# Performance work log

Hardware: AMD Instinct MI355X
Metric: run time of the kernel (lower is better)

The kernel has to match this reference:

```python
import jax, jax.numpy as jnp
import numpy as np

D_MODEL = 1024
NHEAD = 16
HEAD_DIM = D_MODEL // NHEAD
ROPE_BASE = 10000.0


def _rope_freq(T, head_dim):
    half = head_dim // 2
    pos = jnp.arange(T, dtype=jnp.float32)
    idx = jnp.arange(half, dtype=jnp.float32)
    freq_div = ROPE_BASE ** (2.0 * idx / head_dim)
    return pos[:, None] / freq_div[None, :]  # [T, half]


def _rope_rotate(x, cos, sin):
    # x: [B, H, T, d]; cos/sin: [T, d//2]
    half = x.shape[-1] // 2
    xl, xr = x[..., :half], x[..., half:]
    c = cos[None, None]
    s = sin[None, None]
    return jnp.concatenate([xl * c - xr * s, xl * s + xr * c], axis=-1)


def setup_inputs() -> dict:
    key = jax.random.key(0)
    ks = jax.random.split(key, 12)
    B, T = 2, 2048
    sd = 1.0 / np.sqrt(D_MODEL)
    inp = {
        "query": jax.random.normal(ks[0], (B, T, D_MODEL), jnp.float32),
        "key": jax.random.normal(ks[1], (B, T, D_MODEL), jnp.float32),
        "value": jax.random.normal(ks[2], (B, T, D_MODEL), jnp.float32),
        "frac": jax.random.uniform(ks[3], (B, T), jnp.float32),
        # Linear weights stored [in, out] (torch W.T)
        "Wq": jax.random.normal(ks[4], (D_MODEL, D_MODEL), jnp.float32) * sd,
        "Wk": jax.random.normal(ks[5], (D_MODEL, D_MODEL), jnp.float32) * sd,
        "Wv": jax.random.normal(ks[6], (D_MODEL, D_MODEL), jnp.float32) * sd,
        "Wo": jax.random.normal(ks[7], (D_MODEL, D_MODEL), jnp.float32) * sd,
        "bq": jnp.zeros((D_MODEL,), jnp.float32),
        "bk": jnp.zeros((D_MODEL,), jnp.float32),
        "bv": jnp.zeros((D_MODEL,), jnp.float32),
        "bo": jnp.zeros((D_MODEL,), jnp.float32),
        "alpha_pos": jax.random.normal(ks[8], (NHEAD,), jnp.float32) * 0.1,
        "alpha_neg": jax.random.normal(ks[9], (NHEAD,), jnp.float32) * 0.1,
    }
    return inp


def reference(query, key, value, frac, Wq, Wk, Wv, Wo, bq, bk, bv, bo, alpha_pos, alpha_neg):
    B, T, dm = query.shape
    H, hd = NHEAD, HEAD_DIM
    scale = hd ** -0.5

    def split_heads(x):  # [B,T,dm] -> [B,H,T,hd]
        return x.reshape(B, T, H, hd).transpose(0, 2, 1, 3)

    Q = split_heads(query @ Wq + bq)
    K = split_heads(key @ Wk + bk)
    V = split_heads(value @ Wv + bv)

    freq = _rope_freq(T, hd)
    cos, sin = jnp.cos(freq), jnp.sin(freq)
    Q = _rope_rotate(Q, cos, sin)
    K = _rope_rotate(K, cos, sin)

    scores = jnp.einsum("bhqd,bhkd->bhqk", Q, K) * scale  # [B,H,T,T]

    # data-dependent stoichiometric bias
    D = frac[:, None, :] - frac[:, :, None]  # [B,T,T], D[b,i,j] = frac_j - frac_i
    D_pos = jax.nn.relu(D)
    D_neg = -jax.nn.relu(-D)
    bias = (alpha_pos[None, :, None, None] * D_pos[:, None] +
            alpha_neg[None, :, None, None] * D_neg[:, None])  # [B,H,T,T]
    scores = scores + bias

    probs = jax.nn.softmax(scores, axis=-1)
    out = jnp.einsum("bhqk,bhkd->bhqd", probs, V)  # [B,H,T,hd]
    out = out.transpose(0, 2, 1, 3).reshape(B, T, dm)
    return out @ Wo + bo
```

## Files before the change

kernel.cpp:

```cpp
#include <hip/hip_runtime.h>


typedef unsigned short u16;
typedef __bf16 bf8v __attribute__((ext_vector_type(8)));
typedef __bf16 bf4v __attribute__((ext_vector_type(4)));
typedef float f32x4 __attribute__((ext_vector_type(4)));

#define D_MODEL 1024
#define T_SEQ   2048
#define NHEAD   16
#define HDIM    64
#define BATCH   2
#define M_TOT   (BATCH * T_SEQ)
#define LOG2E   1.4426950408889634f

__device__ __forceinline__ void gl2lds16(const u16* g, u16* l) {
  __builtin_amdgcn_global_load_lds(
      (__attribute__((address_space(1))) void*)g,
      (__attribute__((address_space(3))) void*)l, 16, 0, 0);
}

__global__ __launch_bounds__(256) void k_convert_x(
    const float* __restrict__ q, const float* __restrict__ k,
    const float* __restrict__ v, u16* __restrict__ out) {
  int z = blockIdx.y;
  const float* src = (z == 0) ? q : (z == 1) ? k : v;
  u16* dst = out + (size_t)z * (M_TOT * D_MODEL);
  int idx = (blockIdx.x * 256 + threadIdx.x) * 8;
  float4 a = *(const float4*)(src + idx);
  float4 b = *(const float4*)(src + idx + 4);
  bf8v o;
  o[0] = (__bf16)a.x; o[1] = (__bf16)a.y; o[2] = (__bf16)a.z; o[3] = (__bf16)a.w;
  o[4] = (__bf16)b.x; o[5] = (__bf16)b.y; o[6] = (__bf16)b.z; o[7] = (__bf16)b.w;
  *(bf8v*)(dst + idx) = o;
}

__global__ __launch_bounds__(256) void k_rope_table(float* __restrict__ ct,
                                                    float* __restrict__ st) {
  int idx = blockIdx.x * 256 + threadIdx.x;
  int t = idx >> 5, d = idx & 31;
  float ang = (float)t * powf(10000.0f, -(float)d * (1.0f / 32.0f));
  ct[idx] = cosf(ang);
  st[idx] = sinf(ang);
}

__global__ __launch_bounds__(256) void k_transpose_w(
    const float* __restrict__ Wq, const float* __restrict__ Wk,
    const float* __restrict__ Wv, const float* __restrict__ Wo,
    u16* __restrict__ WtB) {
  int z = blockIdx.z;
  const float* W = (z == 0) ? Wq : (z == 1) ? Wk : (z == 2) ? Wv : Wo;
  u16* Wt = WtB + (size_t)z * (D_MODEL * D_MODEL);
  __shared__ float tile[64 * 65];
  int n0 = blockIdx.x * 64, k0 = blockIdx.y * 64;
  int tid = threadIdx.x;
#pragma unroll
  for (int i = 0; i < 16; i++) {
    int idx = tid + i * 256;
    int r = idx >> 6, c = idx & 63;
    tile[c * 65 + r] = W[(size_t)(k0 + r) * D_MODEL + n0 + c];
  }
  __syncthreads();
#pragma unroll
  for (int i = 0; i < 16; i++) {
    int idx = tid + i * 256;
    int r = idx >> 6, c = idx & 63;
    ((__bf16*)Wt)[(size_t)(n0 + r) * D_MODEL + k0 + c] = (__bf16)tile[r * 65 + c];
  }
}

template <int BN>
__device__ __forceinline__ void gemm_core_t(const u16* __restrict__ A,
                                            const u16* __restrict__ Bt,
                                            u16* sA, u16* sB,
                                            f32x4 (&acc)[4][BN / 32],
                                            int m0, int n0) {
  const int K = D_MODEL;
  const int PB = BN * 32;
  int tid = threadIdx.x;
  int lane = tid & 63, wave = tid >> 6;
  int l15 = lane & 15, quad = lane >> 4;
  int wm = (wave >> 1) * 64, wn = (wave & 1) * (BN / 2);
  int r0 = tid >> 2, pcol0 = (tid & 3) * 8;
  int r1 = 64 + r0;
  const u16* A0 = A + (size_t)(m0 + r0) * K + pcol0;
  const u16* A1 = A + (size_t)(m0 + r1) * K + pcol0;
  const u16* B0 = Bt + (size_t)(n0 + r0) * K + pcol0;
  const u16* B1 = Bt + (size_t)(n0 + r1) * K + pcol0;
  u16* dA0 = sA + wave * 512;
  u16* dA1 = sA + 2048 + wave * 512;
  u16* dB0 = sB + wave * 512;
  u16* dB1 = sB + 2048 + wave * 512;
  for (int k0 = 0; k0 < K; k0 += 64) {
    __syncthreads();
    gl2lds16(A0 + k0, dA0);
    gl2lds16(A1 + k0, dA1);
    gl2lds16(A0 + k0 + 32, dA0 + 4096);
    gl2lds16(A1 + k0 + 32, dA1 + 4096);
    gl2lds16(B0 + k0, dB0);
    gl2lds16(B0 + k0 + 32, dB0 + PB);
    if (BN == 128) {
      gl2lds16(B1 + k0, dB1);
      gl2lds16(B1 + k0 + 32, dB1 + PB);
    }
    __syncthreads();
#pragma unroll
    for (int kh = 0; kh < 2; kh++) {
      bf8v af[4], bf[BN / 32];
#pragma unroll
      for (int i = 0; i < 4; i++)
        af[i] = *(const bf8v*)(sA + kh * 4096 + (wm + i * 16 + l15) * 32 + quad * 8);
#pragma unroll
      for (int i = 0; i < BN / 32; i++)
        bf[i] = *(const bf8v*)(sB + kh * PB + (wn + i * 16 + l15) * 32 + quad * 8);
#pragma unroll
      for (int mi = 0; mi < 4; mi++)
#pragma unroll
        for (int ni = 0; ni < BN / 32; ni++)
          acc[mi][ni] = __builtin_amdgcn_mfma_f32_16x16x32_bf16(
              af[mi], bf[ni], acc[mi][ni], 0, 0, 0);
    }
  }
}

__global__ __launch_bounds__(256) void k_gemm_qkv(
    const u16* __restrict__ Xb, const u16* __restrict__ WtB,
    const float* __restrict__ bq, const float* __restrict__ bk,
    const float* __restrict__ bv, const float* __restrict__ ctab,
    const float* __restrict__ stab, u16* __restrict__ OutB) {
  __shared__ __align__(16) u16 sA[128 * 64];
  __shared__ __align__(16) u16 sB[128 * 64];
  int z = blockIdx.z;
  const u16* A = Xb + (size_t)z * (M_TOT * D_MODEL);
  const u16* Bt = WtB + (size_t)z * (D_MODEL * D_MODEL);
  const float* bias = (z == 0) ? bq : (z == 1) ? bk : bv;
  u16* Out = OutB + (size_t)z * (M_TOT * D_MODEL);
  int m0 = blockIdx.y * 128, n0 = blockIdx.x * 128;
  f32x4 acc[4][4] = {};
  gemm_core_t<128>(A, Bt, sA, sB, acc, m0, n0);

  int tid = threadIdx.x, lane = tid & 63, wave = tid >> 6;
  int l15 = lane & 15, quad = lane >> 4;
  int wm = (wave >> 1) * 64, wn = (wave & 1) * 64;
  float bvv[4];
#pragma unroll
  for (int ni = 0; ni < 4; ni++) bvv[ni] = bias[n0 + wn + ni * 16 + l15];
  bool rope = (z < 2);
  float qs = (z == 0) ? 0.125f * LOG2E : 1.0f;
#pragma unroll
  for (int mi = 0; mi < 4; mi++) {
#pragma unroll
    for (int r = 0; r < 4; r++) {
      int m = m0 + wm + mi * 16 + quad * 4 + r;
      size_t ro = (size_t)m * D_MODEL + n0 + wn;
      if (rope) {
        int tl = m & (T_SEQ - 1);
#pragma unroll
        for (int ni = 0; ni < 2; ni++) {
          int d = ni * 16 + l15;
          float c = ctab[tl * 32 + d], s = stab[tl * 32 + d];
          float xl = acc[mi][ni][r] + bvv[ni];
          float xr = acc[mi][ni + 2][r] + bvv[ni + 2];
          ((__bf16*)Out)[ro + d] = (__bf16)((xl * c - xr * s) * qs);
          ((__bf16*)Out)[ro + d + 32] = (__bf16)((xl * s + xr * c) * qs);
        }
      } else {
#pragma unroll
        for (int ni = 0; ni < 4; ni++)
          ((__bf16*)Out)[ro + ni * 16 + l15] = (__bf16)(acc[mi][ni][r] + bvv[ni]);
      }
    }
  }
}

__global__ __launch_bounds__(256) void k_gemm_out(
    const u16* __restrict__ ctx, const u16* __restrict__ Wot,
    const float* __restrict__ bo, float* __restrict__ Cout) {
  __shared__ __align__(16) u16 sA[128 * 64];
  __shared__ __align__(16) u16 sB[64 * 64];
  int m0 = blockIdx.y * 128, n0 = blockIdx.x * 64;
  f32x4 acc[4][2] = {};
  gemm_core_t<64>(ctx, Wot, sA, sB, acc, m0, n0);
  int tid = threadIdx.x, lane = tid & 63, wave = tid >> 6;
  int l15 = lane & 15, quad = lane >> 4;
  int wm = (wave >> 1) * 64, wn = (wave & 1) * 32;
  float bvv[2];
#pragma unroll
  for (int ni = 0; ni < 2; ni++) bvv[ni] = bo[n0 + wn + ni * 16 + l15];
#pragma unroll
  for (int mi = 0; mi < 4; mi++)
#pragma unroll
    for (int r = 0; r < 4; r++) {
      size_t ro = (size_t)(m0 + wm + mi * 16 + quad * 4 + r) * D_MODEL + n0 + wn;
#pragma unroll
      for (int ni = 0; ni < 2; ni++)
        Cout[ro + ni * 16 + l15] = acc[mi][ni][r] + bvv[ni];
    }
}

__global__ __launch_bounds__(256) void k_v_transpose(const u16* __restrict__ Vtmp,
                                                     u16* __restrict__ Vb) {
  int bh = blockIdx.y;
  int b = bh >> 4, h = bh & 15;
  int t0 = blockIdx.x * 64;
  __shared__ u16 st[64 * 65];
  int tid = threadIdx.x;
#pragma unroll
  for (int i = 0; i < 16; i++) {
    int idx = tid + i * 256;
    int tt = idx >> 6, d = idx & 63;
    st[d * 65 + tt] = Vtmp[(size_t)(b * T_SEQ + t0 + tt) * D_MODEL + h * HDIM + d];
  }
  __syncthreads();
#pragma unroll
  for (int i = 0; i < 16; i++) {
    int idx = tid + i * 256;
    int d = idx >> 6, tt = idx & 63;
    Vb[((size_t)bh * HDIM + d) * T_SEQ + t0 + tt] = st[d * 65 + tt];
  }
}

__global__ __launch_bounds__(256) void k_attn(
    const u16* __restrict__ Qr, const u16* __restrict__ Kr,
    const u16* __restrict__ Vb, const float* __restrict__ frac,
    const float* __restrict__ alpha_pos, const float* __restrict__ alpha_neg,
    u16* __restrict__ ctx) {
  __shared__ __align__(16) u16 kT[2][64 * 64];
  __shared__ __align__(16) u16 vT[2][64 * 64];
  __shared__ __align__(16) u16 pT[4][2][16 * 72];
  int bh = blockIdx.y, b = bh >> 4, h = bh & 15;
  int q0 = blockIdx.x * 128;
  int tid = threadIdx.x, wave = tid >> 6, lane = tid & 63;
  int l15 = lane & 15, quad = lane >> 4;

  const u16* Kh = Kr + (size_t)b * T_SEQ * D_MODEL + h * HDIM;
  const u16* Vh = Vb + (size_t)bh * HDIM * T_SEQ;
  const float* fb = frac + b * T_SEQ;

  bf8v qf[2][2];
  float fq[2];
#pragma unroll
  for (int g = 0; g < 2; g++) {
    int qrow = q0 + wave * 32 + g * 16 + l15;
    const u16* qbase =
        Qr + (size_t)(b * T_SEQ + qrow) * D_MODEL + h * HDIM + quad * 8;
    qf[g][0] = *(const bf8v*)qbase;
    qf[g][1] = *(const bf8v*)(qbase + 32);
    fq[g] = fb[qrow];
  }
  float ap = alpha_pos[h] * LOG2E, an = alpha_neg[h] * LOG2E;
  bf8v onesv;
#pragma unroll
  for (int j = 0; j < 8; j++) onesv[j] = (__bf16)1.0f;
  f32x4 o[2][4] = {};
  f32x4 o_l[2] = {};
  u16* pw = (u16*)pT[wave];

  int p0 = tid, p1 = 256 + tid;
  int kr0 = p0 >> 3, gc0 = (p0 & 7) ^ (kr0 & 7);
  int kr1 = p1 >> 3, gc1 = (p1 & 7) ^ (kr1 & 7);
  const u16* kg0 = Kh + (size_t)kr0 * D_MODEL + gc0 * 8;
  const u16* kg1 = Kh + (size_t)kr1 * D_MODEL + gc1 * 8;
  const u16* vg0 = Vh + (size_t)kr0 * T_SEQ + gc0 * 8;
  const u16* vg1 = Vh + (size_t)kr1 * T_SEQ + gc1 * 8;
  int woff = wave * 512;

  auto stage = [&](int buf, int kbase) {
    gl2lds16(kg0 + (size_t)kbase * D_MODEL, kT[buf] + woff);
    gl2lds16(kg1 + (size_t)kbase * D_MODEL, kT[buf] + 2048 + woff);
    gl2lds16(vg0 + kbase, vT[buf] + woff);
    gl2lds16(vg1 + kbase, vT[buf] + 2048 + woff);
  };

  stage(0, 0);
  __syncthreads();

  for (int kt = 0; kt < T_SEQ / 64; kt++) {
    int kbase = kt * 64;
    int buf = kt & 1;
    if (kt + 1 < T_SEQ / 64) stage(buf ^ 1, kbase + 64);

    bf8v kf0[4], kf1[4];
    int x0 = (quad ^ (l15 & 7)) * 8;
#pragma unroll
    for (int nt = 0; nt < 4; nt++) {
      const u16* rb = kT[buf] + ((nt * 16 + l15) << 6);
      kf0[nt] = *(const bf8v*)(rb + x0);
      kf1[nt] = *(const bf8v*)(rb + (x0 ^ 32));
    }
    bf8v vf[2][4];
#pragma unroll
    for (int dt = 0; dt < 4; dt++) {
      const u16* rb = vT[buf] + ((dt * 16 + l15) << 6);
      vf[0][dt] = *(const bf8v*)(rb + x0);
      vf[1][dt] = *(const bf8v*)(rb + (x0 ^ 32));
    }
    f32x4 fk4[4];
#pragma unroll
    for (int nt = 0; nt < 4; nt++)
      fk4[nt] = *(const f32x4*)(fb + kbase + nt * 16 + quad * 4);

#pragma unroll
    for (int g = 0; g < 2; g++) {
      float fqg = fq[g];
      u16* pwg = pw + g * (16 * 72);
#pragma unroll
      for (int nt = 0; nt < 4; nt++) {
        f32x4 s = {};
        s = __builtin_amdgcn_mfma_f32_16x16x32_bf16(kf0[nt], qf[g][0], s, 0, 0, 0);
        s = __builtin_amdgcn_mfma_f32_16x16x32_bf16(kf1[nt], qf[g][1], s, 0, 0, 0);
        bf4v pk;
#pragma unroll
        for (int r = 0; r < 4; r++) {
          float dd = fk4[nt][r] - fqg;
          float sel = (dd >= 0.0f) ? ap : an;
          float p = __builtin_amdgcn_exp2f(fmaf(dd, sel, s[r]));
          pk[r] = (__bf16)p;
        }
        *(bf4v*)(pwg + l15 * 72 + nt * 16 + quad * 4) = pk;
      }
    }
    asm volatile("s_waitcnt lgkmcnt(0)" ::: "memory");

#pragma unroll
    for (int g = 0; g < 2; g++) {
      u16* pwg = pw + g * (16 * 72);
#pragma unroll
      for (int kc = 0; kc < 2; kc++) {
        bf8v pf = *(const bf8v*)(pwg + l15 * 72 + kc * 32 + quad * 8);
        o_l[g] = __builtin_amdgcn_mfma_f32_16x16x32_bf16(pf, onesv, o_l[g], 0, 0, 0);
#pragma unroll
        for (int dt = 0; dt < 4; dt++)
          o[g][dt] = __builtin_amdgcn_mfma_f32_16x16x32_bf16(pf, vf[kc][dt],
                                                             o[g][dt], 0, 0, 0);
      }
    }
    __syncthreads();
  }

#pragma unroll
  for (int g = 0; g < 2; g++) {
#pragma unroll
    for (int r = 0; r < 4; r++) {
      float linv = 1.0f / o_l[g][r];
      int qg = q0 + wave * 32 + g * 16 + quad * 4 + r;
      __bf16* orow = (__bf16*)(ctx + (size_t)(b * T_SEQ + qg) * D_MODEL + h * HDIM);
#pragma unroll
      for (int dt = 0; dt < 4; dt++)
        orow[dt * 16 + l15] = (__bf16)(o[g][dt][r] * linv);
    }
  }
}

extern "C" void kernel_launch(void* const* d_in, const int* in_sizes, int n_in,
                              void* d_out, int out_size, void* d_ws,
                              size_t ws_size, hipStream_t stream) {
  const float* q = (const float*)d_in[0];
  const float* k = (const float*)d_in[1];
  const float* v = (const float*)d_in[2];
  const float* frac = (const float*)d_in[3];
  const float* Wq = (const float*)d_in[4];
  const float* Wk = (const float*)d_in[5];
  const float* Wv = (const float*)d_in[6];
  const float* Wo = (const float*)d_in[7];
  const float* bq = (const float*)d_in[8];
  const float* bk = (const float*)d_in[9];
  const float* bv = (const float*)d_in[10];
  const float* bo = (const float*)d_in[11];
  const float* alpha_pos = (const float*)d_in[12];
  const float* alpha_neg = (const float*)d_in[13];

  char* ws = (char*)d_ws;
  u16* Xb = (u16*)(ws + 0);
  u16* Wt = (u16*)(ws + 25165824);
  u16* Qr = (u16*)(ws + 33554432);
  u16* Kr = (u16*)(ws + 41943040);
  u16* Vtmp = (u16*)(ws + 50331648);
  u16* Vb = (u16*)(ws + 58720256);
  float* ctab = (float*)(ws + 67108864);
  float* stab = (float*)(ws + 67371008);
  u16* ctx = Vtmp;
  u16* QKVout = Qr;

  k_convert_x<<<dim3(2048, 3), 256, 0, stream>>>(q, k, v, Xb);
  k_rope_table<<<dim3(256), 256, 0, stream>>>(ctab, stab);
  k_transpose_w<<<dim3(16, 16, 4), 256, 0, stream>>>(Wq, Wk, Wv, Wo, Wt);
  k_gemm_qkv<<<dim3(8, 32, 3), 256, 0, stream>>>(Xb, Wt, bq, bk, bv, ctab, stab,
                                                 QKVout);
  k_v_transpose<<<dim3(32, 32), 256, 0, stream>>>(Vtmp, Vb);
  k_attn<<<dim3(16, 32), 256, 0, stream>>>(Qr, Kr, Vb, frac, alpha_pos,
                                           alpha_neg, ctx);
  k_gemm_out<<<dim3(16, 32), 256, 0, stream>>>(ctx, Wt + 3 * 1048576, bo,
                                               (float*)d_out);
}
```

Baseline: 268.9 us.

## Merge prep kernels, double-buffer GEMM loads, fuse V transpose, shrink attention P buffer

Folds the input conversion, weight transpose and RoPE table kernels into one launch. The GEMM core is rewritten to double-buffer 32-wide K slices with async global-to-LDS loads, so the next slice's fetch overlaps the current slice's MFMAs and each step needs only one barrier. The V projection epilogue now writes V directly in the transposed per-head layout, which removes the separate transpose kernel but produces strided, uncoalesced 2-byte stores. The attention kernel uses one P scratch tile per wave instead of two, which adds an extra LDS wait per query group.

New measurement: 275.1 us. +2.3%, slower.

```diff
diff --git a/kernel.cpp b/kernel.cpp
--- a/kernel.cpp
+++ b/kernel.cpp
@@ -20,106 +20,104 @@
       (__attribute__((address_space(3))) void*)l, 16, 0, 0);
 }
 
-__global__ __launch_bounds__(256) void k_convert_x(
+__global__ __launch_bounds__(256) void k_prep(
     const float* __restrict__ q, const float* __restrict__ k,
-    const float* __restrict__ v, u16* __restrict__ out) {
-  int z = blockIdx.y;
-  const float* src = (z == 0) ? q : (z == 1) ? k : v;
-  u16* dst = out + (size_t)z * (M_TOT * D_MODEL);
-  int idx = (blockIdx.x * 256 + threadIdx.x) * 8;
-  float4 a = *(const float4*)(src + idx);
-  float4 b = *(const float4*)(src + idx + 4);
-  bf8v o;
-  o[0] = (__bf16)a.x; o[1] = (__bf16)a.y; o[2] = (__bf16)a.z; o[3] = (__bf16)a.w;
-  o[4] = (__bf16)b.x; o[5] = (__bf16)b.y; o[6] = (__bf16)b.z; o[7] = (__bf16)b.w;
-  *(bf8v*)(dst + idx) = o;
-}
-
-__global__ __launch_bounds__(256) void k_rope_table(float* __restrict__ ct,
-                                                    float* __restrict__ st) {
-  int idx = blockIdx.x * 256 + threadIdx.x;
-  int t = idx >> 5, d = idx & 31;
-  float ang = (float)t * powf(10000.0f, -(float)d * (1.0f / 32.0f));
-  ct[idx] = cosf(ang);
-  st[idx] = sinf(ang);
-}
-
-__global__ __launch_bounds__(256) void k_transpose_w(
-    const float* __restrict__ Wq, const float* __restrict__ Wk,
-    const float* __restrict__ Wv, const float* __restrict__ Wo,
-    u16* __restrict__ WtB) {
-  int z = blockIdx.z;
-  const float* W = (z == 0) ? Wq : (z == 1) ? Wk : (z == 2) ? Wv : Wo;
-  u16* Wt = WtB + (size_t)z * (D_MODEL * D_MODEL);
+    const float* __restrict__ v, const float* __restrict__ Wq,
+    const float* __restrict__ Wk, const float* __restrict__ Wv,
+    const float* __restrict__ Wo, u16* __restrict__ Xb, u16* __restrict__ WtB,
+    float* __restrict__ ct, float* __restrict__ st) {
   __shared__ float tile[64 * 65];
-  int n0 = blockIdx.x * 64, k0 = blockIdx.y * 64;
-  int tid = threadIdx.x;
-#pragma unroll
-  for (int i = 0; i < 16; i++) {
-    int idx = tid + i * 256;
-    int r = idx >> 6, c = idx & 63;
-    tile[c * 65 + r] = W[(size_t)(k0 + r) * D_MODEL + n0 + c];
-  }
-  __syncthreads();
-#pragma unroll
-  for (int i = 0; i < 16; i++) {
-    int idx = tid + i * 256;
-    int r = idx >> 6, c = idx & 63;
-    ((__bf16*)Wt)[(size_t)(n0 + r) * D_MODEL + k0 + c] = (__bf16)tile[r * 65 + c];
+  int bx = blockIdx.x, tid = threadIdx.x;
+  if (bx < 6144) {
+    int z = bx >> 11, xb = bx & 2047;
+    const float* src = (z == 0) ? q : (z == 1) ? k : v;
+    u16* dst = Xb + (size_t)z * (M_TOT * D_MODEL);
+    int idx = (xb * 256 + tid) * 8;
+    float4 a = *(const float4*)(src + idx);
+    float4 b = *(const float4*)(src + idx + 4);
+    bf8v o;
+    o[0] = (__bf16)a.x; o[1] = (__bf16)a.y; o[2] = (__bf16)a.z; o[3] = (__bf16)a.w;
+    o[4] = (__bf16)b.x; o[5] = (__bf16)b.y; o[6] = (__bf16)b.z; o[7] = (__bf16)b.w;
+    *(bf8v*)(dst + idx) = o;
+  } else if (bx < 7168) {
+    int idx2 = bx - 6144;
+    int z = idx2 >> 8, rem = idx2 & 255;
+    int k0 = (rem >> 4) * 64, n0 = (rem & 15) * 64;
+    const float* W = (z == 0) ? Wq : (z == 1) ? Wk : (z == 2) ? Wv : Wo;
+    u16* Wt = WtB + (size_t)z * (D_MODEL * D_MODEL);
+#pragma unroll
+    for (int i = 0; i < 16; i++) {
+      int idx = tid + i * 256;
+      int r = idx >> 6, c = idx & 63;
+      tile[c * 65 + r] = W[(size_t)(k0 + r) * D_MODEL + n0 + c];
+    }
+    __syncthreads();
+#pragma unroll
+    for (int i = 0; i < 16; i++) {
+      int idx = tid + i * 256;
+      int r = idx >> 6, c = idx & 63;
+      ((__bf16*)Wt)[(size_t)(n0 + r) * D_MODEL + k0 + c] = (__bf16)tile[r * 65 + c];
+    }
+  } else {
+    int idx = (bx - 7168) * 256 + tid;
+    int t = idx >> 5, d = idx & 31;
+    float ang = (float)t * powf(10000.0f, -(float)d * (1.0f / 32.0f));
+    ct[idx] = cosf(ang);
+    st[idx] = sinf(ang);
   }
 }
 
 template <int BN>
-__device__ __forceinline__ void gemm_core_t(const u16* __restrict__ A,
-                                            const u16* __restrict__ Bt,
-                                            u16* sA, u16* sB,
-                                            f32x4 (&acc)[4][BN / 32],
-                                            int m0, int n0) {
+__device__ __forceinline__ void gemm_core_db(const u16* __restrict__ A,
+                                             const u16* __restrict__ Bt,
+                                             u16* sA, u16* sB,
+                                             f32x4 (&acc)[4][BN / 32],
+                                             int m0, int n0) {
   const int K = D_MODEL;
-  const int PB = BN * 32;
   int tid = threadIdx.x;
   int lane = tid & 63, wave = tid >> 6;
   int l15 = lane & 15, quad = lane >> 4;
   int wm = (wave >> 1) * 64, wn = (wave & 1) * (BN / 2);
-  int r0 = tid >> 2, pcol0 = (tid & 3) * 8;
-  int r1 = 64 + r0;
-  const u16* A0 = A + (size_t)(m0 + r0) * K + pcol0;
-  const u16* A1 = A + (size_t)(m0 + r1) * K + pcol0;
-  const u16* B0 = Bt + (size_t)(n0 + r0) * K + pcol0;
-  const u16* B1 = Bt + (size_t)(n0 + r1) * K + pcol0;
+  int arow = tid >> 2, acol = (tid & 3) * 8;
+  const u16* Ap0 = A + (size_t)(m0 + arow) * K + acol;
+  const u16* Ap1 = Ap0 + (size_t)64 * K;
+  const u16* Bp0 = Bt + (size_t)(n0 + arow) * K + acol;
+  const u16* Bp1 = Bp0 + (size_t)64 * K;
   u16* dA0 = sA + wave * 512;
   u16* dA1 = sA + 2048 + wave * 512;
   u16* dB0 = sB + wave * 512;
   u16* dB1 = sB + 2048 + wave * 512;
-  for (int k0 = 0; k0 < K; k0 += 64) {
+
+  auto stage = [&](int buf, int k0) {
+    int oa = buf * (128 * 32);
+    int ob = buf * (BN * 32);
+    gl2lds16(Ap0 + k0, dA0 + oa);
+    gl2lds16(Ap1 + k0, dA1 + oa);
+    gl2lds16(Bp0 + k0, dB0 + ob);
+    if (BN == 128) gl2lds16(Bp1 + k0, dB1 + ob);
+  };
+
+  stage(0, 0);
+  __syncthreads();
+  for (int k0 = 0; k0 < K; k0 += 32) {
+    int buf = (k0 >> 5) & 1;
+    if (k0 + 32 < K) stage(buf ^ 1, k0 + 32);
+    const u16* bA = sA + buf * (128 * 32);
+    const u16* bB = sB + buf * (BN * 32);
+    bf8v af[4], bf[BN / 32];
+#pragma unroll
+    for (int i = 0; i < 4; i++)
+      af[i] = *(const bf8v*)(bA + (wm + i * 16 + l15) * 32 + quad * 8);
+#pragma unroll
+    for (int i = 0; i < BN / 32; i++)
+      bf[i] = *(const bf8v*)(bB + (wn + i * 16 + l15) * 32 + quad * 8);
+#pragma unroll
+    for (int mi = 0; mi < 4; mi++)
+#pragma unroll
+      for (int ni = 0; ni < BN / 32; ni++)
+        acc[mi][ni] = __builtin_amdgcn_mfma_f32_16x16x32_bf16(
+            af[mi], bf[ni], acc[mi][ni], 0, 0, 0);
     __syncthreads();
-    gl2lds16(A0 + k0, dA0);
-    gl2lds16(A1 + k0, dA1);
-    gl2lds16(A0 + k0 + 32, dA0 + 4096);
-    gl2lds16(A1 + k0 + 32, dA1 + 4096);
-    gl2lds16(B0 + k0, dB0);
-    gl2lds16(B0 + k0 + 32, dB0 + PB);
-    if (BN == 128) {
-      gl2lds16(B1 + k0, dB1);
-      gl2lds16(B1 + k0 + 32, dB1 + PB);
-    }
-    __syncthreads();
-#pragma unroll
-    for (int kh = 0; kh < 2; kh++) {
-      bf8v af[4], bf[BN / 32];
-#pragma unroll
-      for (int i = 0; i < 4; i++)
-        af[i] = *(const bf8v*)(sA + kh * 4096 + (wm + i * 16 + l15) * 32 + quad * 8);
-#pragma unroll
-      for (int i = 0; i < BN / 32; i++)
-        bf[i] = *(const bf8v*)(sB + kh * PB + (wn + i * 16 + l15) * 32 + quad * 8);
-#pragma unroll
-      for (int mi = 0; mi < 4; mi++)
-#pragma unroll
-        for (int ni = 0; ni < BN / 32; ni++)
-          acc[mi][ni] = __builtin_amdgcn_mfma_f32_16x16x32_bf16(
-              af[mi], bf[ni], acc[mi][ni], 0, 0, 0);
-    }
   }
 }
 
@@ -127,9 +125,10 @@
     const u16* __restrict__ Xb, const u16* __restrict__ WtB,
     const float* __restrict__ bq, const float* __restrict__ bk,
     const float* __restrict__ bv, const float* __restrict__ ctab,
-    const float* __restrict__ stab, u16* __restrict__ OutB) {
-  __shared__ __align__(16) u16 sA[128 * 64];
-  __shared__ __align__(16) u16 sB[128 * 64];
+    const float* __restrict__ stab, u16* __restrict__ OutB,
+    u16* __restrict__ Vb) {
+  __shared__ __align__(16) u16 sA[2][128 * 32];
+  __shared__ __align__(16) u16 sB[2][128 * 32];
   int z = blockIdx.z;
   const u16* A = Xb + (size_t)z * (M_TOT * D_MODEL);
   const u16* Bt = WtB + (size_t)z * (D_MODEL * D_MODEL);
@@ -137,7 +136,7 @@
   u16* Out = OutB + (size_t)z * (M_TOT * D_MODEL);
   int m0 = blockIdx.y * 128, n0 = blockIdx.x * 128;
   f32x4 acc[4][4] = {};
-  gemm_core_t<128>(A, Bt, sA, sB, acc, m0, n0);
+  gemm_core_db<128>(A, Bt, &sA[0][0], &sB[0][0], acc, m0, n0);
 
   int tid = threadIdx.x, lane = tid & 63, wave = tid >> 6;
   int l15 = lane & 15, quad = lane >> 4;
@@ -145,15 +144,15 @@
   float bvv[4];
 #pragma unroll
   for (int ni = 0; ni < 4; ni++) bvv[ni] = bias[n0 + wn + ni * 16 + l15];
-  bool rope = (z < 2);
-  float qs = (z == 0) ? 0.125f * LOG2E : 1.0f;
-#pragma unroll
-  for (int mi = 0; mi < 4; mi++) {
-#pragma unroll
-    for (int r = 0; r < 4; r++) {
-      int m = m0 + wm + mi * 16 + quad * 4 + r;
-      size_t ro = (size_t)m * D_MODEL + n0 + wn;
-      if (rope) {
+
+  if (z < 2) {
+    float qs = (z == 0) ? 0.125f * LOG2E : 1.0f;
+#pragma unroll
+    for (int mi = 0; mi < 4; mi++) {
+#pragma unroll
+      for (int r = 0; r < 4; r++) {
+        int m = m0 + wm + mi * 16 + quad * 4 + r;
+        size_t ro = (size_t)m * D_MODEL + n0 + wn;
         int tl = m & (T_SEQ - 1);
 #pragma unroll
         for (int ni = 0; ni < 2; ni++) {
@@ -164,23 +163,36 @@
           ((__bf16*)Out)[ro + d] = (__bf16)((xl * c - xr * s) * qs);
           ((__bf16*)Out)[ro + d + 32] = (__bf16)((xl * s + xr * c) * qs);
         }
-      } else {
-#pragma unroll
-        for (int ni = 0; ni < 4; ni++)
-          ((__bf16*)Out)[ro + ni * 16 + l15] = (__bf16)(acc[mi][ni][r] + bvv[ni]);
       }
     }
+  } else {
+    int hh = (n0 + wn) >> 6;
+    int mbase = m0 + wm;
+    int bb = mbase >> 11;
+    int tbase = mbase & (T_SEQ - 1);
+    u16* Vw = Vb + (size_t)(bb * NHEAD + hh) * HDIM * T_SEQ;
+#pragma unroll
+    for (int mi = 0; mi < 4; mi++)
+#pragma unroll
+      for (int r = 0; r < 4; r++) {
+        int t = tbase + mi * 16 + quad * 4 + r;
+#pragma unroll
+        for (int ni = 0; ni < 4; ni++) {
+          int d = ni * 16 + l15;
+          ((__bf16*)Vw)[(size_t)d * T_SEQ + t] = (__bf16)(acc[mi][ni][r] + bvv[ni]);
+        }
+      }
   }
 }
 
 __global__ __launch_bounds__(256) void k_gemm_out(
     const u16* __restrict__ ctx, const u16* __restrict__ Wot,
     const float* __restrict__ bo, float* __restrict__ Cout) {
-  __shared__ __align__(16) u16 sA[128 * 64];
-  __shared__ __align__(16) u16 sB[64 * 64];
+  __shared__ __align__(16) u16 sA[2][128 * 32];
+  __shared__ __align__(16) u16 sB[2][64 * 32];
   int m0 = blockIdx.y * 128, n0 = blockIdx.x * 64;
   f32x4 acc[4][2] = {};
-  gemm_core_t<64>(ctx, Wot, sA, sB, acc, m0, n0);
+  gemm_core_db<64>(ctx, Wot, &sA[0][0], &sB[0][0], acc, m0, n0);
   int tid = threadIdx.x, lane = tid & 63, wave = tid >> 6;
   int l15 = lane & 15, quad = lane >> 4;
   int wm = (wave >> 1) * 64, wn = (wave & 1) * 32;
@@ -196,28 +208,6 @@
       for (int ni = 0; ni < 2; ni++)
         Cout[ro + ni * 16 + l15] = acc[mi][ni][r] + bvv[ni];
     }
-}
-
-__global__ __launch_bounds__(256) void k_v_transpose(const u16* __restrict__ Vtmp,
-                                                     u16* __restrict__ Vb) {
-  int bh = blockIdx.y;
-  int b = bh >> 4, h = bh & 15;
-  int t0 = blockIdx.x * 64;
-  __shared__ u16 st[64 * 65];
-  int tid = threadIdx.x;
-#pragma unroll
-  for (int i = 0; i < 16; i++) {
-    int idx = tid + i * 256;
-    int tt = idx >> 6, d = idx & 63;
-    st[d * 65 + tt] = Vtmp[(size_t)(b * T_SEQ + t0 + tt) * D_MODEL + h * HDIM + d];
-  }
-  __syncthreads();
-#pragma unroll
-  for (int i = 0; i < 16; i++) {
-    int idx = tid + i * 256;
-    int d = idx >> 6, tt = idx & 63;
-    Vb[((size_t)bh * HDIM + d) * T_SEQ + t0 + tt] = st[d * 65 + tt];
-  }
 }
 
 __global__ __launch_bounds__(256) void k_attn(
@@ -227,7 +217,7 @@
     u16* __restrict__ ctx) {
   __shared__ __align__(16) u16 kT[2][64 * 64];
   __shared__ __align__(16) u16 vT[2][64 * 64];
-  __shared__ __align__(16) u16 pT[4][2][16 * 72];
+  __shared__ __align__(16) u16 pT[4][16 * 72];
   int bh = blockIdx.y, b = bh >> 4, h = bh & 15;
   int q0 = blockIdx.x * 128;
   int tid = threadIdx.x, wave = tid >> 6, lane = tid & 63;
@@ -303,7 +293,6 @@
 #pragma unroll
     for (int g = 0; g < 2; g++) {
       float fqg = fq[g];
-      u16* pwg = pw + g * (16 * 72);
 #pragma unroll
       for (int nt = 0; nt < 4; nt++) {
         f32x4 s = {};
@@ -317,17 +306,12 @@
           float p = __builtin_amdgcn_exp2f(fmaf(dd, sel, s[r]));
           pk[r] = (__bf16)p;
         }
-        *(bf4v*)(pwg + l15 * 72 + nt * 16 + quad * 4) = pk;
+        *(bf4v*)(pw + l15 * 72 + nt * 16 + quad * 4) = pk;
       }
-    }
-    asm volatile("s_waitcnt lgkmcnt(0)" ::: "memory");
-
-#pragma unroll
-    for (int g = 0; g < 2; g++) {
-      u16* pwg = pw + g * (16 * 72);
+      asm volatile("s_waitcnt lgkmcnt(0)" ::: "memory");
 #pragma unroll
       for (int kc = 0; kc < 2; kc++) {
-        bf8v pf = *(const bf8v*)(pwg + l15 * 72 + kc * 32 + quad * 8);
+        bf8v pf = *(const bf8v*)(pw + l15 * 72 + kc * 32 + quad * 8);
         o_l[g] = __builtin_amdgcn_mfma_f32_16x16x32_bf16(pf, onesv, o_l[g], 0, 0, 0);
 #pragma unroll
         for (int dt = 0; dt < 4; dt++)
@@ -382,12 +366,10 @@
   u16* ctx = Vtmp;
   u16* QKVout = Qr;
 
-  k_convert_x<<<dim3(2048, 3), 256, 0, stream>>>(q, k, v, Xb);
-  k_rope_table<<<dim3(256), 256, 0, stream>>>(ctab, stab);
-  k_transpose_w<<<dim3(16, 16, 4), 256, 0, stream>>>(Wq, Wk, Wv, Wo, Wt);
+  k_prep<<<dim3(7424), 256, 0, stream>>>(q, k, v, Wq, Wk, Wv, Wo, Xb, Wt, ctab,
+                                         stab);
   k_gemm_qkv<<<dim3(8, 32, 3), 256, 0, stream>>>(Xb, Wt, bq, bk, bv, ctab, stab,
-                                                 QKVout);
-  k_v_transpose<<<dim3(32, 32), 256, 0, stream>>>(Vtmp, Vb);
+                                                 QKVout, Vb);
   k_attn<<<dim3(16, 32), 256, 0, stream>>>(Qr, Kr, Vb, frac, alpha_pos,
                                            alpha_neg, ctx);
   k_gemm_out<<<dim3(16, 32), 256, 0, stream>>>(ctx, Wt + 3 * 1048576, bo,
```
